# Performance work log

Measured on AMD Instinct MI355X. Metric: run time of the kernel, lower is better.

The kernel has to match this reference:

```python
import jax, jax.numpy as jnp
import numpy as np

L, E, H, FFE = 4, 512, 8, 512  # layers, embed, heads, ff dim (must equal E for residual)
HD = E // H


def _ln(x, g, b):
    mu = jnp.mean(x, -1, keepdims=True)
    var = jnp.mean((x - mu) ** 2, -1, keepdims=True)
    return (x - mu) / jnp.sqrt(var + 1e-5) * g + b


def setup_inputs() -> dict:
    key = jax.random.key(0)
    ks = jax.random.split(key, 8)
    B, S = 8, 128
    w = lambda k, shape: jax.random.normal(k, shape, jnp.float32) * 0.02
    return {
        "x": jax.random.normal(ks[0], (B, S, E), jnp.float32),
        "Wq": w(ks[1], (L, E, E)), "bq": jnp.zeros((L, E), jnp.float32),
        "Wk": w(ks[2], (L, E, E)), "bk": jnp.zeros((L, E), jnp.float32),
        "Wv": w(ks[3], (L, E, E)), "bv": jnp.zeros((L, E), jnp.float32),
        "Wo": w(ks[4], (L, E, E)), "bo": jnp.zeros((L, E), jnp.float32),
        "Wf": w(ks[5], (L, E, FFE)), "bf": jnp.zeros((L, FFE), jnp.float32),
        "g1": jnp.ones((L, E), jnp.float32), "b1": jnp.zeros((L, E), jnp.float32),
        "g2": jnp.ones((L, FFE), jnp.float32), "b2": jnp.zeros((L, FFE), jnp.float32),
    }


def reference(x, Wq, bq, Wk, bk, Wv, bv, Wo, bo, Wf, bf, g1, b1, g2, b2):
    B, S, _ = x.shape

    def stack(xb, mask):
        # xb: [B,S,E]; mask: [S] bool, True = key position inside current prefix.
        # Non-causal MHA restricted to prefix keys exactly reproduces running
        # the original stack on x[:, :s, :] (query positions beyond the prefix
        # produce values we never read).
        h = xb
        for l in range(L):
            q = (h @ Wq[l] + bq[l]).reshape(B, S, H, HD)
            k = (h @ Wk[l] + bk[l]).reshape(B, S, H, HD)
            v = (h @ Wv[l] + bv[l]).reshape(B, S, H, HD)
            sc = jnp.einsum('bqhd,bkhd->bhqk', q, k) / jnp.sqrt(jnp.float32(HD))
            sc = jnp.where(mask[None, None, None, :], sc, jnp.float32(-1e9))
            a = jax.nn.softmax(sc, axis=-1)
            o = jnp.einsum('bhqk,bkhd->bqhd', a, v).reshape(B, S, E)
            h = _ln(o @ Wo[l] + bo[l] + h, g1[l], b1[l])          # MHA + residual + LN1
            h = _ln(jax.nn.relu(h @ Wf[l] + bf[l]) + h, g2[l], b2[l])  # FF + ReLU + residual + LN2
        return h

    # masks[s-1] selects keys 0..s-1 -> prefix of length s
    masks = jnp.tril(jnp.ones((S, S), bool))
    outs = jax.vmap(stack, in_axes=(None, 0))(x, masks)  # [S, B, S, E]
    idx = jnp.arange(S)
    last = outs[idx, :, idx]  # [S, B, E]: last valid token of each prefix run
    return jnp.transpose(last, (1, 0, 2))  # [B, S, E]
```

## Files before the change

### kernel.cpp

```cpp
#include <hip/hip_runtime.h>
#include <stdint.h>

typedef unsigned short u16;
typedef __attribute__((ext_vector_type(8))) short bf16x8;
typedef __attribute__((ext_vector_type(4))) float f32x4;

#define EE 512
#define NH 8
#define HDm 64
#define SS 128
#define NB 8
#define NL 4
#define QKVW 1536

__device__ __forceinline__ float bf2f(u16 v){ union{uint32_t u; float f;} c; c.u=((uint32_t)v)<<16; return c.f; }
__device__ __forceinline__ u16 f2bf(float f){ union{float f; uint32_t u;} c; c.f=f; uint32_t u=c.u; return (u16)((u + 0x7FFFu + ((u>>16)&1u))>>16); }

__device__ __forceinline__ f32x4 mfma16(bf16x8 a, bf16x8 b, f32x4 c){
  return __builtin_amdgcn_mfma_f32_16x16x32_bf16(a,b,c,0,0,0);
}

__device__ __forceinline__ void gload16(const u16* g, u16* l){
  auto gp = reinterpret_cast<const __attribute__((address_space(1))) uint32_t*>(reinterpret_cast<uintptr_t>(g));
  auto lp = reinterpret_cast<__attribute__((address_space(3))) uint32_t*>(reinterpret_cast<uintptr_t>(l));
  __builtin_amdgcn_global_load_lds(gp, lp, 16, 0, 0);
}

#define ABAR() asm volatile("s_barrier" ::: "memory")
#define SB0()  __builtin_amdgcn_sched_barrier(0)

__device__ __forceinline__ void run_map(int bid, int cb, int U, int& r, int& u){
  int rr = 0;
  for (;;){
    int g = (cb + rr) >> 4;
    int gend = ((g + 1) << 4) - cb;
    int upr = (g + 1) * U;
    int span = (gend - rr) * upr;
    if (bid < span){ r = rr + bid / upr; u = bid % upr; return; }
    bid -= span; rr = gend;
  }
}

__global__ __launch_bounds__(256) void wtransT(const float* __restrict__ W, u16* __restrict__ dst,
                                               int dstL, int dstOff){
  __shared__ float tl[32][33];
  int l = blockIdx.y;
  int tile = blockIdx.x;
  int ot = tile & 15, it = tile >> 4;
  int t = threadIdx.x;
  int c = t & 31, r = t >> 5;
  #pragma unroll
  for (int k=0;k<4;k++){
    int ri = it*32 + r + k*8;
    tl[c][r + k*8] = W[(size_t)l*262144 + (size_t)ri*512 + ot*32 + c];
  }
  __syncthreads();
  #pragma unroll
  for (int k=0;k<4;k++){
    int ro = ot*32 + r + k*8;
    dst[(size_t)l*dstL + (size_t)(dstOff + ro)*512 + it*32 + c] = f2bf(tl[r + k*8][c]);
  }
}

__global__ __launch_bounds__(256) void bfuse(const float* __restrict__ bq, const float* __restrict__ bk,
                                             const float* __restrict__ bv, float* __restrict__ bqkv){
  int i = blockIdx.x*256 + threadIdx.x;
  int l = i / QKVW, n = i % QKVW;
  const float* b = (n < 512) ? bq : ((n < 1024) ? bk : bv);
  bqkv[i] = b[l*EE + (n & 511)];
}

__global__ __launch_bounds__(256) void hinit(const float* __restrict__ x, u16* __restrict__ h0){
  int i = (blockIdx.x*256 + threadIdx.x)*8;
  int e = i & 511;
  int pb = i >> 9;
  int b = pb & 7, pp = pb >> 3;
  const float* xp = x + (((size_t)b*SS + pp)<<9) + e;
  union{ bf16x8 v; u16 u[8]; } r;
  #pragma unroll
  for (int j=0;j<8;j++) r.u[j] = f2bf(xp[j]);
  *(bf16x8*)(h0 + i) = r.v;
}

template<int MODE>
__global__ __launch_bounds__(256) void gemm_bt(const u16* __restrict__ A, const u16* __restrict__ Bt,
                                               const float* __restrict__ bias, const u16* __restrict__ res,
                                               u16* __restrict__ o0, u16* __restrict__ o1, u16* __restrict__ o2,
                                               int cb, size_t res_mask){
  __shared__ u16 As[2][128*64];
  __shared__ u16 Bs[2][128*64];
  int t = threadIdx.x;
  int T = gridDim.x, NY = gridDim.y;
  int tile_idx, yb;
  if ((T & 7) == 0){
    int hw = blockIdx.y * T + blockIdx.x;
    int xcd = hw & 7, u = hw >> 3;
    yb = u % NY;
    tile_idx = (u / NY) * 8 + xcd;
  } else { tile_idx = blockIdx.x; yb = blockIdx.y; }
  size_t m0;
  if (cb < 0){
    m0 = (size_t)tile_idx * 128;
  } else {
    int r, tile; run_map(tile_idx, cb, 1, r, tile);
    m0 = (size_t)r*1024 + (size_t)tile*128;
  }
  int n0 = yb*128;
  int wid=t>>6, lane=t&63;
  int wm=wid>>1, wn=wid&1, lr=lane&15, lq=lane>>4;
  f32x4 acc[4][4] = {};
  int srow = t>>3;
  int cg = (t&7) ^ (srow&7);
  const u16* gA = A + (m0+(size_t)srow)*EE + cg*8;
  const u16* gB = Bt + ((size_t)(n0+srow))*EE + cg*8;

  auto stage = [&](int kt, int slot){
    int k0 = kt*64;
    u16* lA = As[slot] + t*8;
    u16* lB = Bs[slot] + t*8;
    #pragma unroll
    for (int j=0;j<4;j++){
      gload16(gA + (size_t)j*32*EE + k0, lA + j*2048);
      gload16(gB + (size_t)j*32*EE + k0, lB + j*2048);
    }
  };

  stage(0,0); stage(1,1);

  #pragma unroll
  for (int kt=0; kt<8; kt++){
    int slot = kt & 1;
    if (kt < 7) asm volatile("s_waitcnt vmcnt(8)" ::: "memory");
    else        asm volatile("s_waitcnt vmcnt(0)" ::: "memory");
    ABAR();
    bf16x8 a[4][2], b[4][2];
    #pragma unroll
    for (int mi=0;mi<4;mi++){
      int row = wm*64 + mi*16 + lr;
      #pragma unroll
      for (int kk=0;kk<2;kk++){
        int c = (kk*4 + lq) ^ (row&7);
        a[mi][kk] = *(const bf16x8*)(As[slot] + row*64 + c*8);
      }
    }
    #pragma unroll
    for (int ni=0;ni<4;ni++){
      int row = wn*64 + ni*16 + lr;
      #pragma unroll
      for (int kk=0;kk<2;kk++){
        int c = (kk*4 + lq) ^ (row&7);
        b[ni][kk] = *(const bf16x8*)(Bs[slot] + row*64 + c*8);
      }
    }
    asm volatile("s_waitcnt lgkmcnt(0)" ::: "memory");
    SB0();
    ABAR();
    if (kt < 6) stage(kt+2, slot);
    #pragma unroll
    for (int mi=0;mi<4;mi++)
      #pragma unroll
      for (int ni=0;ni<4;ni++){
        acc[mi][ni] = mfma16(a[mi][0], b[ni][0], acc[mi][ni]);
        acc[mi][ni] = mfma16(a[mi][1], b[ni][1], acc[mi][ni]);
      }
  }

  int g4 = lane>>4;
  u16* outp;
  int nb;
  if (MODE==0){ int sel = n0 >> 9; outp = sel==0 ? o0 : (sel==1 ? o1 : o2); nb = n0 & 511; }
  else        { outp = o0; nb = n0; }
  #pragma unroll
  for (int ni=0;ni<4;ni++){
    int coln = wn*64 + ni*16 + lr;
    float bv = bias[n0 + coln];
    int col = nb + coln;
    #pragma unroll
    for (int mi=0;mi<4;mi++){
      #pragma unroll
      for (int j=0;j<4;j++){
        size_t row = m0 + (size_t)(wm*64 + mi*16 + g4*4 + j);
        float v = acc[mi][ni][j] + bv;
        if (MODE==2) v = fmaxf(v, 0.f);
        if (MODE>=1) v += bf2f(res[(row & res_mask)*EE + col]);
        outp[row*EE + col] = f2bf(v);
      }
    }
  }
}

__global__ __launch_bounds__(256) void attn(const u16* __restrict__ Q, const u16* __restrict__ K,
                                            const u16* __restrict__ V, u16* __restrict__ Oq,
                                            int cb, int shared_qkv){
  __shared__ u16 Ks[128*72];
  __shared__ u16 Vt[64*136];
  __shared__ u16 Ps[4][16*136];
  int t = threadIdx.x;
  int idx = blockIdx.x;
  int hh = idx & 7, b = (idx>>3)&7, r = idx>>6;
  int m_run = cb + r;
  const size_t RS = (size_t)SS*NB*EE;
  size_t rbase = shared_qkv ? 0 : (size_t)r*RS;
  size_t hb = (size_t)b*EE + hh*HDm;
  size_t obase = (size_t)r*RS + hb;
  int nkc = m_run/32 + 1;
  int nkt = nkc*2;
  int nqt = m_run/16 + 1;
  int nkr = nkt*16;
  for (int i=t; i<nkr*8; i+=256){
    int row=i>>3, c=(i&7)*8;
    *(uint4*)(Ks + row*72 + c) = *(const uint4*)(K + rbase + (size_t)row*NB*EE + hb + c);
  }
  for (int i=t; i<nkr*8; i+=256){
    int row=i>>3, c=(i&7)*8;
    uint4 raw = *(const uint4*)(V + rbase + (size_t)row*NB*EE + hb + c);
    const u16* pv = (const u16*)&raw;
    #pragma unroll
    for (int j=0;j<8;j++) Vt[(c+j)*136 + row] = pv[j];
  }
  __syncthreads();
  int wid=t>>6, lane=t&63, lr=lane&15, g=lane>>4, lk=(lane>>4)*8;
  u16* Pw = Ps[wid];
  for (int iq=0; iq<2; iq++){
    int qt = wid*2 + iq;
    if (qt >= nqt) continue;
    const u16* qrow = Q + rbase + (size_t)(qt*16+lr)*NB*EE + hb;
    bf16x8 qa0 = *(const bf16x8*)(qrow + lk);
    bf16x8 qa1 = *(const bf16x8*)(qrow + 32 + lk);
    f32x4 sc[8];
    #pragma unroll
    for (int kt=0;kt<8;kt++){
      if (kt < nkt){
        f32x4 c = {};
        bf16x8 kb0 = *(const bf16x8*)(Ks + (kt*16+lr)*72 + lk);
        bf16x8 kb1 = *(const bf16x8*)(Ks + (kt*16+lr)*72 + 32 + lk);
        c = mfma16(qa0, kb0, c);
        c = mfma16(qa1, kb1, c);
        int key = kt*16 + lr;
        #pragma unroll
        for (int i2=0;i2<4;i2++)
          sc[kt][i2] = (key <= m_run) ? c[i2]*0.125f : -1e9f;
      }
    }
    #pragma unroll
    for (int i2=0;i2<4;i2++){
      float v = -3.0e38f;
      #pragma unroll
      for (int kt=0;kt<8;kt++) if (kt<nkt) v = fmaxf(v, sc[kt][i2]);
      v = fmaxf(v, __shfl_xor(v,1));
      v = fmaxf(v, __shfl_xor(v,2));
      v = fmaxf(v, __shfl_xor(v,4));
      v = fmaxf(v, __shfl_xor(v,8));
      float s = 0.f;
      #pragma unroll
      for (int kt=0;kt<8;kt++) if (kt<nkt){ float e2=__expf(sc[kt][i2]-v); sc[kt][i2]=e2; s+=e2; }
      s += __shfl_xor(s,1); s += __shfl_xor(s,2); s += __shfl_xor(s,4); s += __shfl_xor(s,8);
      float inv = 1.f/s;
      #pragma unroll
      for (int kt=0;kt<8;kt++) if (kt<nkt) sc[kt][i2] *= inv;
    }
    #pragma unroll
    for (int kt=0;kt<8;kt++) if (kt<nkt){
      #pragma unroll
      for (int i2=0;i2<4;i2++)
        Pw[(g*4+i2)*136 + kt*16 + lr] = f2bf(sc[kt][i2]);
    }
    f32x4 oa[4] = {};
    #pragma unroll
    for (int kc=0;kc<4;kc++) if (kc<nkc){
      bf16x8 pa = *(const bf16x8*)(Pw + lr*136 + kc*32 + lk);
      #pragma unroll
      for (int dt=0;dt<4;dt++){
        bf16x8 vb = *(const bf16x8*)(Vt + (dt*16+lr)*136 + kc*32 + lk);
        oa[dt] = mfma16(pa, vb, oa[dt]);
      }
    }
    #pragma unroll
    for (int dt=0;dt<4;dt++){
      #pragma unroll
      for (int j=0;j<4;j++){
        size_t prow = (size_t)(qt*16 + g*4 + j);
        Oq[obase + prow*NB*EE + dt*16 + lr] = f2bf(oa[dt][j]);
      }
    }
  }
}

__global__ __launch_bounds__(256) void lnorm(const u16* __restrict__ in, const float* __restrict__ gg,
                                             const float* __restrict__ bb, u16* __restrict__ outp, int cb){
  int r, u; run_map(blockIdx.x, cb, 8, r, u);
  int lane = threadIdx.x & 63;
  float gv[8], bv2[8];
  #pragma unroll
  for (int j=0;j<8;j++){ gv[j] = gg[lane*8+j]; bv2[j] = bb[lane*8+j]; }
  #pragma unroll
  for (int it=0; it<4; it++){
    size_t row = (size_t)r*1024 + (size_t)u*16 + it*4 + (threadIdx.x>>6);
    const u16* p = in + row*EE + lane*8;
    union{ bf16x8 v; u16 u[8]; } d; d.v = *(const bf16x8*)p;
    float f[8]; float s=0.f;
    #pragma unroll
    for (int j=0;j<8;j++){ f[j]=bf2f(d.u[j]); s+=f[j]; }
    #pragma unroll
    for (int o=1;o<64;o<<=1) s += __shfl_xor(s,o);
    float mu = s*(1.f/512.f);
    float s2=0.f;
    #pragma unroll
    for (int j=0;j<8;j++){ float tt=f[j]-mu; s2+=tt*tt; }
    #pragma unroll
    for (int o=1;o<64;o<<=1) s2 += __shfl_xor(s2,o);
    float rstd = rsqrtf(s2*(1.f/512.f)+1e-5f);
    union{ bf16x8 v; u16 u[8]; } rr;
    #pragma unroll
    for (int j=0;j<8;j++) rr.u[j] = f2bf((f[j]-mu)*rstd*gv[j] + bv2[j]);
    *(bf16x8*)(outp + row*EE + lane*8) = rr.v;
  }
}

__global__ __launch_bounds__(256) void extract(const u16* __restrict__ h, float* __restrict__ out, int cb){
  int i = blockIdx.x*256 + threadIdx.x;
  int e = i & 511;
  int b = (i >> 9) & 7;
  int r = i >> 12;
  int m = cb + r;
  out[((size_t)b*SS + m)*EE + e] = bf2f(h[(((size_t)r*SS + m)*NB + b)*EE + e]);
}

extern "C" void kernel_launch(void* const* d_in, const int* in_sizes, int n_in,
                              void* d_out, int out_size, void* d_ws, size_t ws_size,
                              hipStream_t stream){
  const float* x   = (const float*)d_in[0];
  const float* Wq  = (const float*)d_in[1];
  const float* bq  = (const float*)d_in[2];
  const float* Wk  = (const float*)d_in[3];
  const float* bk  = (const float*)d_in[4];
  const float* Wv  = (const float*)d_in[5];
  const float* bv  = (const float*)d_in[6];
  const float* Wo  = (const float*)d_in[7];
  const float* bo  = (const float*)d_in[8];
  const float* Wf  = (const float*)d_in[9];
  const float* bfb = (const float*)d_in[10];
  const float* g1  = (const float*)d_in[11];
  const float* b1  = (const float*)d_in[12];
  const float* g2  = (const float*)d_in[13];
  const float* b2  = (const float*)d_in[14];
  float* out = (float*)d_out;

  uint8_t* p = (uint8_t*)d_ws;
  u16* WqkvT = (u16*)p; p += (size_t)NL*QKVW*EE*2;
  u16* WoT   = (u16*)p; p += (size_t)NL*EE*EE*2;
  u16* WfT   = (u16*)p; p += (size_t)NL*EE*EE*2;
  float* bqkv= (float*)p; p += (size_t)NL*QKVW*4;
  u16* h0    = (u16*)p; p += (size_t)SS*NB*EE*2;
  u16* q0    = (u16*)p; p += (size_t)SS*NB*EE*2;
  u16* k0    = (u16*)p; p += (size_t)SS*NB*EE*2;
  u16* v0    = (u16*)p; p += (size_t)SS*NB*EE*2;
  size_t used = (size_t)(p - (uint8_t*)d_ws);

  int RC = 128;
  const size_t PER_RUN = (size_t)SS*NB*EE*2*5;
  while (RC > 1 && used + (size_t)RC*PER_RUN > ws_size) RC >>= 1;

  const size_t BUF = (size_t)RC*SS*NB*EE*2;
  u16* h   = (u16*)p; p += BUF;
  u16* q   = (u16*)p; p += BUF;
  u16* k   = (u16*)p; p += BUF;
  u16* v   = (u16*)p; p += BUF;
  u16* tmp = (u16*)p; p += BUF;

  const size_t NOMASK = ~(size_t)0;
  const int QL = QKVW*EE;
  const int OL = EE*EE;

  wtransT<<<dim3(256,NL),256,0,stream>>>(Wq, WqkvT, QL, 0);
  wtransT<<<dim3(256,NL),256,0,stream>>>(Wk, WqkvT, QL, 512);
  wtransT<<<dim3(256,NL),256,0,stream>>>(Wv, WqkvT, QL, 1024);
  wtransT<<<dim3(256,NL),256,0,stream>>>(Wo, WoT, OL, 0);
  wtransT<<<dim3(256,NL),256,0,stream>>>(Wf, WfT, OL, 0);
  bfuse<<<24,256,0,stream>>>(bq, bk, bv, bqkv);
  hinit<<<256,256,0,stream>>>(x, h0);
  gemm_bt<0><<<dim3(8,12),256,0,stream>>>(h0, WqkvT, bqkv, nullptr, q0, k0, v0, -1, 0);

  for (int cb=0; cb<SS; cb+=RC){
    int t128 = 0;
    for (int r2=0;r2<RC;r2++) t128 += (cb+r2)/16 + 1;

    attn<<<dim3(RC*64),256,0,stream>>>(q0, k0, v0, q, cb, 1);
    gemm_bt<1><<<dim3(t128,4),256,0,stream>>>(q, WoT, bo, h0, tmp, tmp, tmp, cb, (size_t)1023);
    lnorm<<<dim3(t128*8),256,0,stream>>>(tmp, g1, b1, h, cb);
    gemm_bt<2><<<dim3(t128,4),256,0,stream>>>(h, WfT, bfb, h, tmp, tmp, tmp, cb, NOMASK);
    lnorm<<<dim3(t128*8),256,0,stream>>>(tmp, g2, b2, h, cb);

    for (int l=1;l<NL;l++){
      gemm_bt<0><<<dim3(t128,12),256,0,stream>>>(h, WqkvT+(size_t)l*QL, bqkv+l*QKVW, nullptr, q, k, v, cb, 0);
      attn<<<dim3(RC*64),256,0,stream>>>(q, k, v, q, cb, 0);
      gemm_bt<1><<<dim3(t128,4),256,0,stream>>>(q, WoT+(size_t)l*OL, bo+l*EE, h, tmp, tmp, tmp, cb, NOMASK);
      lnorm<<<dim3(t128*8),256,0,stream>>>(tmp, g1+l*EE, b1+l*EE, h, cb);
      gemm_bt<2><<<dim3(t128,4),256,0,stream>>>(h, WfT+(size_t)l*OL, bfb+l*EE, h, tmp, tmp, tmp, cb, NOMASK);
      lnorm<<<dim3(t128*8),256,0,stream>>>(tmp, g2+l*EE, b2+l*EE, h, cb);
    }
    extract<<<dim3(RC*16),256,0,stream>>>(h, out, cb);
  }
}
```

Baseline: 1.868 ms.

## Fuse per-layer kernel sequence into one cooperative persistent megakernel with grid syncs

Replaces the chain of attention, GEMM and layernorm launches per chunk with one cooperative persistent kernel that loops over stages and separates them with grid-wide syncs. The GEMM and attention bodies become device functions sharing dynamic LDS. The goal is to remove launch overhead and inter-kernel gaps across the many small launches. The cost is a fixed grid of 256 or 512 blocks, which may load-balance worse than the old right-sized grids, plus the latency of each grid sync. A fallback to the old multi-launch path remains for when cooperative launch fails.

Measured after the change: 6.390 ms. 3.42x slower.

```diff
diff --git a/kernel.cpp b/kernel.cpp
--- a/kernel.cpp
+++ b/kernel.cpp
@@ -1,5 +1,8 @@
 #include <hip/hip_runtime.h>
+#include <hip/hip_cooperative_groups.h>
 #include <stdint.h>
+
+namespace cg = cooperative_groups;
 
 typedef unsigned short u16;
 typedef __attribute__((ext_vector_type(8))) short bf16x8;
@@ -41,63 +44,13 @@
   }
 }
 
-__global__ __launch_bounds__(256) void wtransT(const float* __restrict__ W, u16* __restrict__ dst,
-                                               int dstL, int dstOff){
-  __shared__ float tl[32][33];
-  int l = blockIdx.y;
-  int tile = blockIdx.x;
-  int ot = tile & 15, it = tile >> 4;
+
+__device__ __forceinline__ void gemm_unit(const u16* __restrict__ A, const u16* __restrict__ Bt,
+                                          const float* __restrict__ bias, const u16* __restrict__ res,
+                                          u16* __restrict__ o0, u16* __restrict__ o1, u16* __restrict__ o2,
+                                          int cb, size_t res_mask, int mode,
+                                          int tile_idx, int yb, u16* lds){
   int t = threadIdx.x;
-  int c = t & 31, r = t >> 5;
-  #pragma unroll
-  for (int k=0;k<4;k++){
-    int ri = it*32 + r + k*8;
-    tl[c][r + k*8] = W[(size_t)l*262144 + (size_t)ri*512 + ot*32 + c];
-  }
-  __syncthreads();
-  #pragma unroll
-  for (int k=0;k<4;k++){
-    int ro = ot*32 + r + k*8;
-    dst[(size_t)l*dstL + (size_t)(dstOff + ro)*512 + it*32 + c] = f2bf(tl[r + k*8][c]);
-  }
-}
-
-__global__ __launch_bounds__(256) void bfuse(const float* __restrict__ bq, const float* __restrict__ bk,
-                                             const float* __restrict__ bv, float* __restrict__ bqkv){
-  int i = blockIdx.x*256 + threadIdx.x;
-  int l = i / QKVW, n = i % QKVW;
-  const float* b = (n < 512) ? bq : ((n < 1024) ? bk : bv);
-  bqkv[i] = b[l*EE + (n & 511)];
-}
-
-__global__ __launch_bounds__(256) void hinit(const float* __restrict__ x, u16* __restrict__ h0){
-  int i = (blockIdx.x*256 + threadIdx.x)*8;
-  int e = i & 511;
-  int pb = i >> 9;
-  int b = pb & 7, pp = pb >> 3;
-  const float* xp = x + (((size_t)b*SS + pp)<<9) + e;
-  union{ bf16x8 v; u16 u[8]; } r;
-  #pragma unroll
-  for (int j=0;j<8;j++) r.u[j] = f2bf(xp[j]);
-  *(bf16x8*)(h0 + i) = r.v;
-}
-
-template<int MODE>
-__global__ __launch_bounds__(256) void gemm_bt(const u16* __restrict__ A, const u16* __restrict__ Bt,
-                                               const float* __restrict__ bias, const u16* __restrict__ res,
-                                               u16* __restrict__ o0, u16* __restrict__ o1, u16* __restrict__ o2,
-                                               int cb, size_t res_mask){
-  __shared__ u16 As[2][128*64];
-  __shared__ u16 Bs[2][128*64];
-  int t = threadIdx.x;
-  int T = gridDim.x, NY = gridDim.y;
-  int tile_idx, yb;
-  if ((T & 7) == 0){
-    int hw = blockIdx.y * T + blockIdx.x;
-    int xcd = hw & 7, u = hw >> 3;
-    yb = u % NY;
-    tile_idx = (u / NY) * 8 + xcd;
-  } else { tile_idx = blockIdx.x; yb = blockIdx.y; }
   size_t m0;
   if (cb < 0){
     m0 = (size_t)tile_idx * 128;
@@ -110,14 +63,16 @@
   int wm=wid>>1, wn=wid&1, lr=lane&15, lq=lane>>4;
   f32x4 acc[4][4] = {};
   int srow = t>>3;
-  int cg = (t&7) ^ (srow&7);
-  const u16* gA = A + (m0+(size_t)srow)*EE + cg*8;
-  const u16* gB = Bt + ((size_t)(n0+srow))*EE + cg*8;
+  int cg2 = (t&7) ^ (srow&7);
+  const u16* gA = A + (m0+(size_t)srow)*EE + cg2*8;
+  const u16* gB = Bt + ((size_t)(n0+srow))*EE + cg2*8;
+  u16* As0 = lds;
+  u16* Bs0 = lds + 16384;
 
   auto stage = [&](int kt, int slot){
     int k0 = kt*64;
-    u16* lA = As[slot] + t*8;
-    u16* lB = Bs[slot] + t*8;
+    u16* lA = As0 + slot*8192 + t*8;
+    u16* lB = Bs0 + slot*8192 + t*8;
     #pragma unroll
     for (int j=0;j<4;j++){
       gload16(gA + (size_t)j*32*EE + k0, lA + j*2048);
@@ -140,7 +95,7 @@
       #pragma unroll
       for (int kk=0;kk<2;kk++){
         int c = (kk*4 + lq) ^ (row&7);
-        a[mi][kk] = *(const bf16x8*)(As[slot] + row*64 + c*8);
+        a[mi][kk] = *(const bf16x8*)(As0 + slot*8192 + row*64 + c*8);
       }
     }
     #pragma unroll
@@ -149,7 +104,7 @@
       #pragma unroll
       for (int kk=0;kk<2;kk++){
         int c = (kk*4 + lq) ^ (row&7);
-        b[ni][kk] = *(const bf16x8*)(Bs[slot] + row*64 + c*8);
+        b[ni][kk] = *(const bf16x8*)(Bs0 + slot*8192 + row*64 + c*8);
       }
     }
     asm volatile("s_waitcnt lgkmcnt(0)" ::: "memory");
@@ -166,9 +121,8 @@
   }
 
   int g4 = lane>>4;
-  u16* outp;
-  int nb;
-  if (MODE==0){ int sel = n0 >> 9; outp = sel==0 ? o0 : (sel==1 ? o1 : o2); nb = n0 & 511; }
+  u16* outp; int nb;
+  if (mode==0){ int sel = n0 >> 9; outp = sel==0 ? o0 : (sel==1 ? o1 : o2); nb = n0 & 511; }
   else        { outp = o0; nb = n0; }
   #pragma unroll
   for (int ni=0;ni<4;ni++){
@@ -181,22 +135,21 @@
       for (int j=0;j<4;j++){
         size_t row = m0 + (size_t)(wm*64 + mi*16 + g4*4 + j);
         float v = acc[mi][ni][j] + bv;
-        if (MODE==2) v = fmaxf(v, 0.f);
-        if (MODE>=1) v += bf2f(res[(row & res_mask)*EE + col]);
+        if (mode==2) v = fmaxf(v, 0.f);
+        if (mode>=1) v += bf2f(res[(row & res_mask)*EE + col]);
         outp[row*EE + col] = f2bf(v);
       }
     }
   }
 }
 
-__global__ __launch_bounds__(256) void attn(const u16* __restrict__ Q, const u16* __restrict__ K,
-                                            const u16* __restrict__ V, u16* __restrict__ Oq,
-                                            int cb, int shared_qkv){
-  __shared__ u16 Ks[128*72];
-  __shared__ u16 Vt[64*136];
-  __shared__ u16 Ps[4][16*136];
+__device__ __forceinline__ void attn_unit(const u16* __restrict__ Q, const u16* __restrict__ K,
+                                          const u16* __restrict__ V, u16* __restrict__ Oq,
+                                          int cb, int shared_qkv, int idx, u16* lds){
+  u16* Ks = lds;
+  u16* Vt = lds + 9216;
+  u16* Ps = lds + 17920;
   int t = threadIdx.x;
-  int idx = blockIdx.x;
   int hh = idx & 7, b = (idx>>3)&7, r = idx>>6;
   int m_run = cb + r;
   const size_t RS = (size_t)SS*NB*EE;
@@ -220,7 +173,7 @@
   }
   __syncthreads();
   int wid=t>>6, lane=t&63, lr=lane&15, g=lane>>4, lk=(lane>>4)*8;
-  u16* Pw = Ps[wid];
+  u16* Pw = Ps + wid*2176;
   for (int iq=0; iq<2; iq++){
     int qt = wid*2 + iq;
     if (qt >= nqt) continue;
@@ -284,6 +237,167 @@
       }
     }
   }
+  __syncthreads();
+}
+
+__device__ __forceinline__ void ln_rows(const u16* __restrict__ in, const float* gv, const float* bv2,
+                                        u16* __restrict__ outp, size_t row){
+  int lane = threadIdx.x & 63;
+  const u16* p = in + row*EE + lane*8;
+  union{ bf16x8 v; u16 u[8]; } d; d.v = *(const bf16x8*)p;
+  float f[8]; float s=0.f;
+  #pragma unroll
+  for (int j=0;j<8;j++){ f[j]=bf2f(d.u[j]); s+=f[j]; }
+  #pragma unroll
+  for (int o=1;o<64;o<<=1) s += __shfl_xor(s,o);
+  float mu = s*(1.f/512.f);
+  float s2=0.f;
+  #pragma unroll
+  for (int j=0;j<8;j++){ float tt=f[j]-mu; s2+=tt*tt; }
+  #pragma unroll
+  for (int o=1;o<64;o<<=1) s2 += __shfl_xor(s2,o);
+  float rstd = rsqrtf(s2*(1.f/512.f)+1e-5f);
+  union{ bf16x8 v; u16 u[8]; } rr;
+  #pragma unroll
+  for (int j=0;j<8;j++) rr.u[j] = f2bf((f[j]-mu)*rstd*gv[j] + bv2[j]);
+  *(bf16x8*)(outp + row*EE + lane*8) = rr.v;
+}
+
+
+struct MegaArgs {
+  const u16 *WqkvT, *WoT, *WfT;
+  const float *bqkv, *bo, *bfb, *g1, *b1, *g2, *b2, *x;
+  u16 *h0, *q0, *k0, *v0;
+  u16 *h, *q, *k, *v, *tmp;
+  float *out;
+  int cb, RC, t128;
+};
+
+__global__ __launch_bounds__(256, 2) void mega(MegaArgs a){
+  extern __shared__ u16 lds[];
+  cg::grid_group grid = cg::this_grid();
+  int G = gridDim.x;
+  int bid = blockIdx.x, t = threadIdx.x;
+  const size_t NOMASK = ~(size_t)0;
+  const size_t QL = (size_t)QKVW*EE, OL = (size_t)EE*EE;
+
+  if (a.cb == 0){
+    for (int i = bid*256 + t; i < SS*NB*EE/8; i += G*256){
+      int ii = i*8;
+      int e = ii & 511;
+      int pb = ii >> 9;
+      int b = pb & 7, pp = pb >> 3;
+      const float* xp = a.x + (((size_t)b*SS + pp)<<9) + e;
+      union{ bf16x8 v; u16 u[8]; } rv;
+      #pragma unroll
+      for (int j=0;j<8;j++) rv.u[j] = f2bf(xp[j]);
+      *(bf16x8*)(a.h0 + ii) = rv.v;
+    }
+    grid.sync();
+    for (int u = bid; u < 96; u += G)
+      gemm_unit(a.h0, a.WqkvT, a.bqkv, nullptr, a.q0, a.k0, a.v0, -1, 0, 0, u/12, u%12, lds);
+    grid.sync();
+  }
+
+  for (int l = 0; l < NL; l++){
+    {
+      int total = a.RC*64;
+      for (int u = bid; u < total; u += G)
+        attn_unit(l==0 ? a.q0 : a.q, l==0 ? a.k0 : a.k, l==0 ? a.v0 : a.v,
+                  a.q, a.cb, l==0 ? 1 : 0, u, lds);
+    }
+    grid.sync();
+    {
+      int total = a.t128*4, per = (total + G - 1)/G;
+      for (int i=0;i<per;i++){
+        int u = bid*per + i;
+        if (u < total)
+          gemm_unit(a.q, a.WoT + (size_t)l*OL, a.bo + l*EE,
+                    l==0 ? a.h0 : a.h, a.tmp, nullptr, nullptr,
+                    a.cb, l==0 ? (size_t)1023 : NOMASK, 1, u/4, u%4, lds);
+      }
+    }
+    grid.sync();
+    {
+      int lane = t & 63;
+      float gv[8], bv2[8];
+      #pragma unroll
+      for (int j=0;j<8;j++){ gv[j] = a.g1[l*EE + lane*8+j]; bv2[j] = a.b1[l*EE + lane*8+j]; }
+      int total = a.t128*32;
+      for (int uu = bid; uu < total; uu += G){
+        int r, u2; run_map(uu, a.cb, 32, r, u2);
+        size_t row = (size_t)r*1024 + (size_t)u2*4 + (t>>6);
+        ln_rows(a.tmp, gv, bv2, a.h, row);
+      }
+    }
+    grid.sync();
+    {
+      int total = a.t128*4, per = (total + G - 1)/G;
+      for (int i=0;i<per;i++){
+        int u = bid*per + i;
+        if (u < total)
+          gemm_unit(a.h, a.WfT + (size_t)l*OL, a.bfb + l*EE,
+                    a.h, a.tmp, nullptr, nullptr,
+                    a.cb, NOMASK, 2, u/4, u%4, lds);
+      }
+    }
+    grid.sync();
+    {
+      int lane = t & 63;
+      float gv[8], bv2[8];
+      #pragma unroll
+      for (int j=0;j<8;j++){ gv[j] = a.g2[l*EE + lane*8+j]; bv2[j] = a.b2[l*EE + lane*8+j]; }
+      int total = a.t128*32;
+      for (int uu = bid; uu < total; uu += G){
+        int r, u2; run_map(uu, a.cb, 32, r, u2);
+        size_t row = (size_t)r*1024 + (size_t)u2*4 + (t>>6);
+        ln_rows(a.tmp, gv, bv2, a.h, row);
+      }
+    }
+    grid.sync();
+    if (l < NL-1){
+      int total = a.t128*12, per = (total + G - 1)/G;
+      for (int i=0;i<per;i++){
+        int u = bid*per + i;
+        if (u < total)
+          gemm_unit(a.h, a.WqkvT + (size_t)(l+1)*QL, a.bqkv + (l+1)*QKVW,
+                    nullptr, a.q, a.k, a.v, a.cb, 0, 0, u/12, u%12, lds);
+      }
+      grid.sync();
+    }
+  }
+  for (int i = bid*256 + t; i < a.RC*NB*EE; i += G*256){
+    int e = i & 511;
+    int b = (i >> 9) & 7;
+    int r = i >> 12;
+    int m = a.cb + r;
+    a.out[((size_t)b*SS + m)*EE + e] = bf2f(a.h[(((size_t)r*SS + m)*NB + b)*EE + e]);
+  }
+}
+
+
+template<int MODE>
+__global__ __launch_bounds__(256) void gemm_bt(const u16* __restrict__ A, const u16* __restrict__ Bt,
+                                               const float* __restrict__ bias, const u16* __restrict__ res,
+                                               u16* __restrict__ o0, u16* __restrict__ o1, u16* __restrict__ o2,
+                                               int cb, size_t res_mask){
+  __shared__ u16 slds[32768];
+  int T = gridDim.x, NY = gridDim.y;
+  int tile_idx, yb;
+  if ((T & 7) == 0){
+    int hw = blockIdx.y * T + blockIdx.x;
+    int xcd = hw & 7, u = hw >> 3;
+    yb = u % NY;
+    tile_idx = (u / NY) * 8 + xcd;
+  } else { tile_idx = blockIdx.x; yb = blockIdx.y; }
+  gemm_unit(A, Bt, bias, res, o0, o1, o2, cb, res_mask, MODE, tile_idx, yb, slds);
+}
+
+__global__ __launch_bounds__(256) void attn_g(const u16* __restrict__ Q, const u16* __restrict__ K,
+                                              const u16* __restrict__ V, u16* __restrict__ Oq,
+                                              int cb, int shared_qkv){
+  __shared__ u16 slds[26624];
+  attn_unit(Q, K, V, Oq, cb, shared_qkv, blockIdx.x, slds);
 }
 
 __global__ __launch_bounds__(256) void lnorm(const u16* __restrict__ in, const float* __restrict__ gg,
@@ -296,24 +410,7 @@
   #pragma unroll
   for (int it=0; it<4; it++){
     size_t row = (size_t)r*1024 + (size_t)u*16 + it*4 + (threadIdx.x>>6);
-    const u16* p = in + row*EE + lane*8;
-    union{ bf16x8 v; u16 u[8]; } d; d.v = *(const bf16x8*)p;
-    float f[8]; float s=0.f;
-    #pragma unroll
-    for (int j=0;j<8;j++){ f[j]=bf2f(d.u[j]); s+=f[j]; }
-    #pragma unroll
-    for (int o=1;o<64;o<<=1) s += __shfl_xor(s,o);
-    float mu = s*(1.f/512.f);
-    float s2=0.f;
-    #pragma unroll
-    for (int j=0;j<8;j++){ float tt=f[j]-mu; s2+=tt*tt; }
-    #pragma unroll
-    for (int o=1;o<64;o<<=1) s2 += __shfl_xor(s2,o);
-    float rstd = rsqrtf(s2*(1.f/512.f)+1e-5f);
-    union{ bf16x8 v; u16 u[8]; } rr;
-    #pragma unroll
-    for (int j=0;j<8;j++) rr.u[j] = f2bf((f[j]-mu)*rstd*gv[j] + bv2[j]);
-    *(bf16x8*)(outp + row*EE + lane*8) = rr.v;
+    ln_rows(in, gv, bv2, outp, row);
   }
 }
 
@@ -325,6 +422,49 @@
   int m = cb + r;
   out[((size_t)b*SS + m)*EE + e] = bf2f(h[(((size_t)r*SS + m)*NB + b)*EE + e]);
 }
+
+__global__ __launch_bounds__(256) void hinit(const float* __restrict__ x, u16* __restrict__ h0){
+  int i = (blockIdx.x*256 + threadIdx.x)*8;
+  int e = i & 511;
+  int pb = i >> 9;
+  int b = pb & 7, pp = pb >> 3;
+  const float* xp = x + (((size_t)b*SS + pp)<<9) + e;
+  union{ bf16x8 v; u16 u[8]; } r;
+  #pragma unroll
+  for (int j=0;j<8;j++) r.u[j] = f2bf(xp[j]);
+  *(bf16x8*)(h0 + i) = r.v;
+}
+
+
+__global__ __launch_bounds__(256) void wtransT(const float* __restrict__ W, u16* __restrict__ dst,
+                                               int dstL, int dstOff){
+  __shared__ float tl[32][33];
+  int l = blockIdx.y;
+  int tile = blockIdx.x;
+  int ot = tile & 15, it = tile >> 4;
+  int t = threadIdx.x;
+  int c = t & 31, r = t >> 5;
+  #pragma unroll
+  for (int k=0;k<4;k++){
+    int ri = it*32 + r + k*8;
+    tl[c][r + k*8] = W[(size_t)l*262144 + (size_t)ri*512 + ot*32 + c];
+  }
+  __syncthreads();
+  #pragma unroll
+  for (int k=0;k<4;k++){
+    int ro = ot*32 + r + k*8;
+    dst[(size_t)l*dstL + (size_t)(dstOff + ro)*512 + it*32 + c] = f2bf(tl[r + k*8][c]);
+  }
+}
+
+__global__ __launch_bounds__(256) void bfuse(const float* __restrict__ bq, const float* __restrict__ bk,
+                                             const float* __restrict__ bv, float* __restrict__ bqkv){
+  int i = blockIdx.x*256 + threadIdx.x;
+  int l = i / QKVW, n = i % QKVW;
+  const float* b = (n < 512) ? bq : ((n < 1024) ? bk : bv);
+  bqkv[i] = b[l*EE + (n & 511)];
+}
+
 
 extern "C" void kernel_launch(void* const* d_in, const int* in_sizes, int n_in,
                               void* d_out, int out_size, void* d_ws, size_t ws_size,
@@ -346,6 +486,8 @@
   const float* b2  = (const float*)d_in[14];
   float* out = (float*)d_out;
 
+  hipFuncSetAttribute((const void*)mega, hipFuncAttributeMaxDynamicSharedMemorySize, 65536);
+
   uint8_t* p = (uint8_t*)d_ws;
   u16* WqkvT = (u16*)p; p += (size_t)NL*QKVW*EE*2;
   u16* WoT   = (u16*)p; p += (size_t)NL*EE*EE*2;
@@ -369,36 +511,61 @@
   u16* tmp = (u16*)p; p += BUF;
 
   const size_t NOMASK = ~(size_t)0;
-  const int QL = QKVW*EE;
-  const int OL = EE*EE;
-
-  wtransT<<<dim3(256,NL),256,0,stream>>>(Wq, WqkvT, QL, 0);
-  wtransT<<<dim3(256,NL),256,0,stream>>>(Wk, WqkvT, QL, 512);
-  wtransT<<<dim3(256,NL),256,0,stream>>>(Wv, WqkvT, QL, 1024);
-  wtransT<<<dim3(256,NL),256,0,stream>>>(Wo, WoT, OL, 0);
-  wtransT<<<dim3(256,NL),256,0,stream>>>(Wf, WfT, OL, 0);
+  const size_t QL = (size_t)QKVW*EE;
+  const size_t OL = (size_t)EE*EE;
+
+  wtransT<<<dim3(256,NL),256,0,stream>>>(Wq, WqkvT, (int)QL, 0);
+  wtransT<<<dim3(256,NL),256,0,stream>>>(Wk, WqkvT, (int)QL, 512);
+  wtransT<<<dim3(256,NL),256,0,stream>>>(Wv, WqkvT, (int)QL, 1024);
+  wtransT<<<dim3(256,NL),256,0,stream>>>(Wo, WoT, (int)OL, 0);
+  wtransT<<<dim3(256,NL),256,0,stream>>>(Wf, WfT, (int)OL, 0);
   bfuse<<<24,256,0,stream>>>(bq, bk, bv, bqkv);
-  hinit<<<256,256,0,stream>>>(x, h0);
-  gemm_bt<0><<<dim3(8,12),256,0,stream>>>(h0, WqkvT, bqkv, nullptr, q0, k0, v0, -1, 0);
-
-  for (int cb=0; cb<SS; cb+=RC){
-    int t128 = 0;
-    for (int r2=0;r2<RC;r2++) t128 += (cb+r2)/16 + 1;
-
-    attn<<<dim3(RC*64),256,0,stream>>>(q0, k0, v0, q, cb, 1);
-    gemm_bt<1><<<dim3(t128,4),256,0,stream>>>(q, WoT, bo, h0, tmp, tmp, tmp, cb, (size_t)1023);
-    lnorm<<<dim3(t128*8),256,0,stream>>>(tmp, g1, b1, h, cb);
-    gemm_bt<2><<<dim3(t128,4),256,0,stream>>>(h, WfT, bfb, h, tmp, tmp, tmp, cb, NOMASK);
-    lnorm<<<dim3(t128*8),256,0,stream>>>(tmp, g2, b2, h, cb);
-
-    for (int l=1;l<NL;l++){
-      gemm_bt<0><<<dim3(t128,12),256,0,stream>>>(h, WqkvT+(size_t)l*QL, bqkv+l*QKVW, nullptr, q, k, v, cb, 0);
-      attn<<<dim3(RC*64),256,0,stream>>>(q, k, v, q, cb, 0);
-      gemm_bt<1><<<dim3(t128,4),256,0,stream>>>(q, WoT+(size_t)l*OL, bo+l*EE, h, tmp, tmp, tmp, cb, NOMASK);
-      lnorm<<<dim3(t128*8),256,0,stream>>>(tmp, g1+l*EE, b1+l*EE, h, cb);
-      gemm_bt<2><<<dim3(t128,4),256,0,stream>>>(h, WfT+(size_t)l*OL, bfb+l*EE, h, tmp, tmp, tmp, cb, NOMASK);
-      lnorm<<<dim3(t128*8),256,0,stream>>>(tmp, g2+l*EE, b2+l*EE, h, cb);
-    }
-    extract<<<dim3(RC*16),256,0,stream>>>(h, out, cb);
-  }
-}
+
+  int coopDev = 0;
+  hipDeviceGetAttribute(&coopDev, hipDeviceAttributeCooperativeLaunch, 0);
+  int occ = 0;
+  hipOccupancyMaxActiveBlocksPerMultiprocessor(&occ, (const void*)mega, 256, 65536);
+  bool useCoop = (coopDev != 0) && (occ >= 1);
+  int G = occ >= 2 ? 512 : 256;
+
+  if (useCoop){
+    for (int cb=0; cb<SS && useCoop; cb+=RC){
+      int t128 = 0;
+      for (int r2=0;r2<RC;r2++) t128 += (cb+r2)/16 + 1;
+      MegaArgs ma;
+      ma.WqkvT=WqkvT; ma.WoT=WoT; ma.WfT=WfT;
+      ma.bqkv=bqkv; ma.bo=bo; ma.bfb=bfb; ma.g1=g1; ma.b1=b1; ma.g2=g2; ma.b2=b2; ma.x=x;
+      ma.h0=h0; ma.q0=q0; ma.k0=k0; ma.v0=v0;
+      ma.h=h; ma.q=q; ma.k=k; ma.v=v; ma.tmp=tmp;
+      ma.out=out; ma.cb=cb; ma.RC=RC; ma.t128=t128;
+      void* kp[] = { (void*)&ma };
+      hipError_t e = hipLaunchCooperativeKernel((const void*)mega, dim3(G), dim3(256), kp, 65536, stream);
+      if (e != hipSuccess) useCoop = false;
+    }
+  }
+
+  if (!useCoop){
+    hinit<<<256,256,0,stream>>>(x, h0);
+    gemm_bt<0><<<dim3(8,12),256,0,stream>>>(h0, WqkvT, bqkv, nullptr, q0, k0, v0, -1, 0);
+    for (int cb=0; cb<SS; cb+=RC){
+      int t128 = 0;
+      for (int r2=0;r2<RC;r2++) t128 += (cb+r2)/16 + 1;
+
+      attn_g<<<dim3(RC*64),256,0,stream>>>(q0, k0, v0, q, cb, 1);
+      gemm_bt<1><<<dim3(t128,4),256,0,stream>>>(q, WoT, bo, h0, tmp, nullptr, nullptr, cb, (size_t)1023);
+      lnorm<<<dim3(t128*8),256,0,stream>>>(tmp, g1, b1, h, cb);
+      gemm_bt<2><<<dim3(t128,4),256,0,stream>>>(h, WfT, bfb, h, tmp, nullptr, nullptr, cb, NOMASK);
+      lnorm<<<dim3(t128*8),256,0,stream>>>(tmp, g2, b2, h, cb);
+
+      for (int l=1;l<NL;l++){
+        gemm_bt<0><<<dim3(t128,12),256,0,stream>>>(h, WqkvT+(size_t)l*QL, bqkv+l*QKVW, nullptr, q, k, v, cb, 0);
+        attn_g<<<dim3(RC*64),256,0,stream>>>(q, k, v, q, cb, 0);
+        gemm_bt<1><<<dim3(t128,4),256,0,stream>>>(q, WoT+(size_t)l*OL, bo+l*EE, h, tmp, nullptr, nullptr, cb, NOMASK);
+        lnorm<<<dim3(t128*8),256,0,stream>>>(tmp, g1+l*EE, b1+l*EE, h, cb);
+        gemm_bt<2><<<dim3(t128,4),256,0,stream>>>(h, WfT+(size_t)l*OL, bfb+l*EE, h, tmp, nullptr, nullptr, cb, NOMASK);
+        lnorm<<<dim3(t128*8),256,0,stream>>>(tmp, g2+l*EE, b2+l*EE, h, cb);
+      }
+      extract<<<dim3(RC*16),256,0,stream>>>(h, out, cb);
+    }
+  }
+}
```

## Fuse LayerNorm and output extraction into GEMM epilogue via last-block atomic counter

Applied to the files above, without the earlier changes.

Removes the separate lnorm and extract kernels. The last of the four N-tile blocks of each row tile, detected with an atomic counter, performs the LayerNorm over the full 128 rows and, on the final layer, writes the output rows. The five weight transposes, the bias fuse and the hinit kernel are also merged into one prep launch. This cuts launch count and a round trip of the pre-LN tensor through separate kernels, but adds a threadfence and atomic per block and serialises the LN work onto one block per row tile.

Result: slower. 5.605 ms (+200.1%).

```diff
diff --git a/kernel.cpp b/kernel.cpp
--- a/kernel.cpp
+++ b/kernel.cpp
@@ -41,52 +41,68 @@
   }
 }
 
-__global__ __launch_bounds__(256) void wtransT(const float* __restrict__ W, u16* __restrict__ dst,
-                                               int dstL, int dstOff){
-  __shared__ float tl[32][33];
-  int l = blockIdx.y;
-  int tile = blockIdx.x;
-  int ot = tile & 15, it = tile >> 4;
+__global__ __launch_bounds__(256) void prep(const float* __restrict__ Wq, const float* __restrict__ Wk,
+                                            const float* __restrict__ Wv, const float* __restrict__ Wo,
+                                            const float* __restrict__ Wf,
+                                            const float* __restrict__ bq, const float* __restrict__ bk,
+                                            const float* __restrict__ bv, const float* __restrict__ x,
+                                            u16* __restrict__ WqkvT, u16* __restrict__ WoT,
+                                            u16* __restrict__ WfT, float* __restrict__ bqkv,
+                                            u16* __restrict__ h0){
+  int bid = blockIdx.x;
   int t = threadIdx.x;
-  int c = t & 31, r = t >> 5;
-  #pragma unroll
-  for (int k=0;k<4;k++){
-    int ri = it*32 + r + k*8;
-    tl[c][r + k*8] = W[(size_t)l*262144 + (size_t)ri*512 + ot*32 + c];
-  }
-  __syncthreads();
-  #pragma unroll
-  for (int k=0;k<4;k++){
-    int ro = ot*32 + r + k*8;
-    dst[(size_t)l*dstL + (size_t)(dstOff + ro)*512 + it*32 + c] = f2bf(tl[r + k*8][c]);
-  }
-}
-
-__global__ __launch_bounds__(256) void bfuse(const float* __restrict__ bq, const float* __restrict__ bk,
-                                             const float* __restrict__ bv, float* __restrict__ bqkv){
-  int i = blockIdx.x*256 + threadIdx.x;
-  int l = i / QKVW, n = i % QKVW;
-  const float* b = (n < 512) ? bq : ((n < 1024) ? bk : bv);
-  bqkv[i] = b[l*EE + (n & 511)];
-}
-
-__global__ __launch_bounds__(256) void hinit(const float* __restrict__ x, u16* __restrict__ h0){
-  int i = (blockIdx.x*256 + threadIdx.x)*8;
-  int e = i & 511;
-  int pb = i >> 9;
-  int b = pb & 7, pp = pb >> 3;
-  const float* xp = x + (((size_t)b*SS + pp)<<9) + e;
-  union{ bf16x8 v; u16 u[8]; } r;
-  #pragma unroll
-  for (int j=0;j<8;j++) r.u[j] = f2bf(xp[j]);
-  *(bf16x8*)(h0 + i) = r.v;
+  if (bid < 5120){
+    __shared__ float tl[32][33];
+    int grp = bid >> 10;
+    int within = bid & 1023;
+    int l = within >> 8, tile = within & 255;
+    const float* W; u16* dst; int dstL, dstOff;
+    switch(grp){
+      case 0: W=Wq; dst=WqkvT; dstL=QKVW*EE; dstOff=0;    break;
+      case 1: W=Wk; dst=WqkvT; dstL=QKVW*EE; dstOff=512;  break;
+      case 2: W=Wv; dst=WqkvT; dstL=QKVW*EE; dstOff=1024; break;
+      case 3: W=Wo; dst=WoT;   dstL=EE*EE;   dstOff=0;    break;
+      default:W=Wf; dst=WfT;   dstL=EE*EE;   dstOff=0;    break;
+    }
+    int ot = tile & 15, it = tile >> 4;
+    int c = t & 31, r = t >> 5;
+    #pragma unroll
+    for (int k=0;k<4;k++){
+      int ri = it*32 + r + k*8;
+      tl[c][r + k*8] = W[(size_t)l*262144 + (size_t)ri*512 + ot*32 + c];
+    }
+    __syncthreads();
+    #pragma unroll
+    for (int k=0;k<4;k++){
+      int ro = ot*32 + r + k*8;
+      dst[(size_t)l*dstL + (size_t)(dstOff + ro)*512 + it*32 + c] = f2bf(tl[r + k*8][c]);
+    }
+  } else if (bid < 5144){
+    int i = (bid - 5120)*256 + t;
+    int l = i / QKVW, n = i % QKVW;
+    const float* b = (n < 512) ? bq : ((n < 1024) ? bk : bv);
+    bqkv[i] = b[l*EE + (n & 511)];
+  } else {
+    int i = ((bid - 5144)*256 + t)*8;
+    int e = i & 511;
+    int pb = i >> 9;
+    int b = pb & 7, pp = pb >> 3;
+    const float* xp = x + (((size_t)b*SS + pp)<<9) + e;
+    union{ bf16x8 v; u16 u[8]; } rv;
+    #pragma unroll
+    for (int j=0;j<8;j++) rv.u[j] = f2bf(xp[j]);
+    *(bf16x8*)(h0 + i) = rv.v;
+  }
 }
 
 template<int MODE>
 __global__ __launch_bounds__(256) void gemm_bt(const u16* __restrict__ A, const u16* __restrict__ Bt,
                                                const float* __restrict__ bias, const u16* __restrict__ res,
                                                u16* __restrict__ o0, u16* __restrict__ o1, u16* __restrict__ o2,
-                                               int cb, size_t res_mask){
+                                               int cb, size_t res_mask,
+                                               const float* __restrict__ lng, const float* __restrict__ lnb,
+                                               u16* __restrict__ lnout, int* cnt,
+                                               float* __restrict__ fout, int last){
   __shared__ u16 As[2][128*64];
   __shared__ u16 Bs[2][128*64];
   int t = threadIdx.x;
@@ -99,20 +115,21 @@
     tile_idx = (u / NY) * 8 + xcd;
   } else { tile_idx = blockIdx.x; yb = blockIdx.y; }
   size_t m0;
+  int rrun = 0, tile16 = 0;
   if (cb < 0){
     m0 = (size_t)tile_idx * 128;
   } else {
-    int r, tile; run_map(tile_idx, cb, 1, r, tile);
-    m0 = (size_t)r*1024 + (size_t)tile*128;
+    run_map(tile_idx, cb, 1, rrun, tile16);
+    m0 = (size_t)rrun*1024 + (size_t)tile16*128;
   }
   int n0 = yb*128;
   int wid=t>>6, lane=t&63;
   int wm=wid>>1, wn=wid&1, lr=lane&15, lq=lane>>4;
   f32x4 acc[4][4] = {};
   int srow = t>>3;
-  int cg = (t&7) ^ (srow&7);
-  const u16* gA = A + (m0+(size_t)srow)*EE + cg*8;
-  const u16* gB = Bt + ((size_t)(n0+srow))*EE + cg*8;
+  int cg2 = (t&7) ^ (srow&7);
+  const u16* gA = A + (m0+(size_t)srow)*EE + cg2*8;
+  const u16* gB = Bt + ((size_t)(n0+srow))*EE + cg2*8;
 
   auto stage = [&](int kt, int slot){
     int k0 = kt*64;
@@ -166,8 +183,7 @@
   }
 
   int g4 = lane>>4;
-  u16* outp;
-  int nb;
+  u16* outp; int nb;
   if (MODE==0){ int sel = n0 >> 9; outp = sel==0 ? o0 : (sel==1 ? o1 : o2); nb = n0 & 511; }
   else        { outp = o0; nb = n0; }
   #pragma unroll
@@ -185,6 +201,52 @@
         if (MODE>=1) v += bf2f(res[(row & res_mask)*EE + col]);
         outp[row*EE + col] = f2bf(v);
       }
+    }
+  }
+
+  if (MODE==1 || MODE==2){
+    __threadfence();
+    __shared__ int lastFlag;
+    __syncthreads();
+    if (t == 0) lastFlag = (atomicAdd(&cnt[tile_idx], 1) == 3) ? 1 : 0;
+    __syncthreads();
+    if (lastFlag){
+      __threadfence();
+      int w = t >> 6;
+      int m_run = cb + rrun;
+      float gv[8], bv2[8];
+      #pragma unroll
+      for (int j=0;j<8;j++){ gv[j] = lng[lane*8+j]; bv2[j] = lnb[lane*8+j]; }
+      for (int it2=0; it2<32; it2++){
+        size_t row = m0 + (size_t)it2*4 + w;
+        const u16* pp = o0 + row*EE + lane*8;
+        union{ bf16x8 v; u16 u[8]; } d; d.v = *(const bf16x8*)pp;
+        float f[8]; float s=0.f;
+        #pragma unroll
+        for (int j=0;j<8;j++){ f[j]=bf2f(d.u[j]); s+=f[j]; }
+        #pragma unroll
+        for (int o=1;o<64;o<<=1) s += __shfl_xor(s,o);
+        float mu = s*(1.f/512.f);
+        float s2=0.f;
+        #pragma unroll
+        for (int j=0;j<8;j++){ float tt=f[j]-mu; s2+=tt*tt; }
+        #pragma unroll
+        for (int o=1;o<64;o<<=1) s2 += __shfl_xor(s2,o);
+        float rstd = rsqrtf(s2*(1.f/512.f)+1e-5f);
+        union{ bf16x8 v; u16 u[8]; } rr;
+        #pragma unroll
+        for (int j=0;j<8;j++) rr.u[j] = f2bf((f[j]-mu)*rstd*gv[j] + bv2[j]);
+        *(bf16x8*)(lnout + row*EE + lane*8) = rr.v;
+        if (MODE==2 && last){
+          int local = tile16*128 + it2*4 + w;
+          int pidx = local >> 3, b3 = local & 7;
+          if (pidx == m_run){
+            #pragma unroll
+            for (int j=0;j<8;j++) fout[((size_t)b3*SS + pidx)*EE + lane*8 + j] = bf2f(rr.u[j]);
+          }
+        }
+      }
+      if (t == 0) cnt[tile_idx] = 0;
     }
   }
 }
@@ -286,46 +348,6 @@
   }
 }
 
-__global__ __launch_bounds__(256) void lnorm(const u16* __restrict__ in, const float* __restrict__ gg,
-                                             const float* __restrict__ bb, u16* __restrict__ outp, int cb){
-  int r, u; run_map(blockIdx.x, cb, 8, r, u);
-  int lane = threadIdx.x & 63;
-  float gv[8], bv2[8];
-  #pragma unroll
-  for (int j=0;j<8;j++){ gv[j] = gg[lane*8+j]; bv2[j] = bb[lane*8+j]; }
-  #pragma unroll
-  for (int it=0; it<4; it++){
-    size_t row = (size_t)r*1024 + (size_t)u*16 + it*4 + (threadIdx.x>>6);
-    const u16* p = in + row*EE + lane*8;
-    union{ bf16x8 v; u16 u[8]; } d; d.v = *(const bf16x8*)p;
-    float f[8]; float s=0.f;
-    #pragma unroll
-    for (int j=0;j<8;j++){ f[j]=bf2f(d.u[j]); s+=f[j]; }
-    #pragma unroll
-    for (int o=1;o<64;o<<=1) s += __shfl_xor(s,o);
-    float mu = s*(1.f/512.f);
-    float s2=0.f;
-    #pragma unroll
-    for (int j=0;j<8;j++){ float tt=f[j]-mu; s2+=tt*tt; }
-    #pragma unroll
-    for (int o=1;o<64;o<<=1) s2 += __shfl_xor(s2,o);
-    float rstd = rsqrtf(s2*(1.f/512.f)+1e-5f);
-    union{ bf16x8 v; u16 u[8]; } rr;
-    #pragma unroll
-    for (int j=0;j<8;j++) rr.u[j] = f2bf((f[j]-mu)*rstd*gv[j] + bv2[j]);
-    *(bf16x8*)(outp + row*EE + lane*8) = rr.v;
-  }
-}
-
-__global__ __launch_bounds__(256) void extract(const u16* __restrict__ h, float* __restrict__ out, int cb){
-  int i = blockIdx.x*256 + threadIdx.x;
-  int e = i & 511;
-  int b = (i >> 9) & 7;
-  int r = i >> 12;
-  int m = cb + r;
-  out[((size_t)b*SS + m)*EE + e] = bf2f(h[(((size_t)r*SS + m)*NB + b)*EE + e]);
-}
-
 extern "C" void kernel_launch(void* const* d_in, const int* in_sizes, int n_in,
                               void* d_out, int out_size, void* d_ws, size_t ws_size,
                               hipStream_t stream){
@@ -355,6 +377,8 @@
   u16* q0    = (u16*)p; p += (size_t)SS*NB*EE*2;
   u16* k0    = (u16*)p; p += (size_t)SS*NB*EE*2;
   u16* v0    = (u16*)p; p += (size_t)SS*NB*EE*2;
+  int* cnt1  = (int*)p; p += 1024*4;
+  int* cnt2  = (int*)p; p += 1024*4;
   size_t used = (size_t)(p - (uint8_t*)d_ws);
 
   int RC = 128;
@@ -369,36 +393,34 @@
   u16* tmp = (u16*)p; p += BUF;
 
   const size_t NOMASK = ~(size_t)0;
-  const int QL = QKVW*EE;
-  const int OL = EE*EE;
-
-  wtransT<<<dim3(256,NL),256,0,stream>>>(Wq, WqkvT, QL, 0);
-  wtransT<<<dim3(256,NL),256,0,stream>>>(Wk, WqkvT, QL, 512);
-  wtransT<<<dim3(256,NL),256,0,stream>>>(Wv, WqkvT, QL, 1024);
-  wtransT<<<dim3(256,NL),256,0,stream>>>(Wo, WoT, OL, 0);
-  wtransT<<<dim3(256,NL),256,0,stream>>>(Wf, WfT, OL, 0);
-  bfuse<<<24,256,0,stream>>>(bq, bk, bv, bqkv);
-  hinit<<<256,256,0,stream>>>(x, h0);
-  gemm_bt<0><<<dim3(8,12),256,0,stream>>>(h0, WqkvT, bqkv, nullptr, q0, k0, v0, -1, 0);
+  const size_t QL = (size_t)QKVW*EE;
+  const size_t OL = (size_t)EE*EE;
+
+  hipMemsetAsync(cnt1, 0, 1024*4, stream);
+  hipMemsetAsync(cnt2, 0, 1024*4, stream);
+  prep<<<5400,256,0,stream>>>(Wq, Wk, Wv, Wo, Wf, bq, bk, bv, x, WqkvT, WoT, WfT, bqkv, h0);
+  gemm_bt<0><<<dim3(8,12),256,0,stream>>>(h0, WqkvT, bqkv, nullptr, q0, k0, v0, -1, 0,
+                                          nullptr, nullptr, nullptr, nullptr, nullptr, 0);
 
   for (int cb=0; cb<SS; cb+=RC){
     int t128 = 0;
     for (int r2=0;r2<RC;r2++) t128 += (cb+r2)/16 + 1;
 
     attn<<<dim3(RC*64),256,0,stream>>>(q0, k0, v0, q, cb, 1);
-    gemm_bt<1><<<dim3(t128,4),256,0,stream>>>(q, WoT, bo, h0, tmp, tmp, tmp, cb, (size_t)1023);
-    lnorm<<<dim3(t128*8),256,0,stream>>>(tmp, g1, b1, h, cb);
-    gemm_bt<2><<<dim3(t128,4),256,0,stream>>>(h, WfT, bfb, h, tmp, tmp, tmp, cb, NOMASK);
-    lnorm<<<dim3(t128*8),256,0,stream>>>(tmp, g2, b2, h, cb);
+    gemm_bt<1><<<dim3(t128,4),256,0,stream>>>(q, WoT, bo, h0, tmp, nullptr, nullptr, cb, (size_t)1023,
+                                              g1, b1, h, cnt1, nullptr, 0);
+    gemm_bt<2><<<dim3(t128,4),256,0,stream>>>(h, WfT, bfb, h, tmp, nullptr, nullptr, cb, NOMASK,
+                                              g2, b2, h, cnt2, out, 0);
 
     for (int l=1;l<NL;l++){
-      gemm_bt<0><<<dim3(t128,12),256,0,stream>>>(h, WqkvT+(size_t)l*QL, bqkv+l*QKVW, nullptr, q, k, v, cb, 0);
+      gemm_bt<0><<<dim3(t128,12),256,0,stream>>>(h, WqkvT+(size_t)l*QL, bqkv+l*QKVW, nullptr, q, k, v,
+                                                 cb, 0, nullptr, nullptr, nullptr, nullptr, nullptr, 0);
       attn<<<dim3(RC*64),256,0,stream>>>(q, k, v, q, cb, 0);
-      gemm_bt<1><<<dim3(t128,4),256,0,stream>>>(q, WoT+(size_t)l*OL, bo+l*EE, h, tmp, tmp, tmp, cb, NOMASK);
-      lnorm<<<dim3(t128*8),256,0,stream>>>(tmp, g1+l*EE, b1+l*EE, h, cb);
-      gemm_bt<2><<<dim3(t128,4),256,0,stream>>>(h, WfT+(size_t)l*OL, bfb+l*EE, h, tmp, tmp, tmp, cb, NOMASK);
-      lnorm<<<dim3(t128*8),256,0,stream>>>(tmp, g2+l*EE, b2+l*EE, h, cb);
-    }
-    extract<<<dim3(RC*16),256,0,stream>>>(h, out, cb);
-  }
-}
+      gemm_bt<1><<<dim3(t128,4),256,0,stream>>>(q, WoT+(size_t)l*OL, bo+l*EE, h, tmp, nullptr, nullptr,
+                                                cb, NOMASK, g1+l*EE, b1+l*EE, h, cnt1, nullptr, 0);
+      gemm_bt<2><<<dim3(t128,4),256,0,stream>>>(h, WfT+(size_t)l*OL, bfb+l*EE, h, tmp, nullptr, nullptr,
+                                                cb, NOMASK, g2+l*EE, b2+l*EE, h, cnt2, out,
+                                                (l==NL-1) ? 1 : 0);
+    }
+  }
+}
```
